# Kernel optimization log

Measured on AMD Instinct MI355X. Metric: run time of the kernel, lower is better.

Reference implementation:

```python
import jax, jax.numpy as jnp
import numpy as np

N, M, D = 65536, 1024, 2

def setup_inputs() -> dict:
    key = jax.random.key(0)
    k1, k2, k3, k4 = jax.random.split(key, 4)
    sample = jax.random.normal(k1, (N, D), dtype=jnp.float32)
    mu = jax.random.uniform(k2, (M, D), dtype=jnp.float32)
    A = jax.random.normal(k3, (M, D, D), dtype=jnp.float32)
    w = jax.random.normal(k4, (M, 1), dtype=jnp.float32)
    return {"sample": sample, "mu": mu, "A": A, "w": w}


def reference(sample, mu, A, w):
    # Covariance-like precision matrices: gamma_j = A_j A_j^T / 2, shape [M, D, D]
    gamma = jnp.matmul(A, jnp.swapaxes(A, 1, 2)) / 2.0
    # Hand-rolled 2x2 determinants (matches covariances_determinants)
    dets = gamma[:, 0, 0] * gamma[:, 1, 1] - gamma[:, 0, 1] * gamma[:, 1, 0]  # [M]
    # log of the scalar factor in front of each Gaussian (weights_log)
    log_w = jax.nn.log_softmax(w, axis=0)[:, 0] + 0.5 * jnp.log(dets)  # [M]
    # Pairwise Mahalanobis quadratic form q_ij = (x_i - mu_j)^T gamma_j (x_i - mu_j)
    diff = sample[:, None, :] - mu[None, :, :]  # [N, M, D]
    q = jnp.einsum('nmd,mde,nme->nm', diff, gamma, diff)  # [N, M]
    # 'lse' mode of kernel_product: log sum_j exp(log_w_j - q_ij)
    ll = jax.scipy.special.logsumexp(log_w[None, :] - q, axis=1)  # [N]
    return ll[:, None]
```

## Files before the change

### kernel.cpp

```cpp
#include <hip/hip_runtime.h>
#include <hip/hip_bf16.h>
#include <math.h>

#define LOG2E 1.4426950408889634f
#define LN2   0.6931471805599453f

typedef float v2f __attribute__((ext_vector_type(2)));

__device__ __forceinline__ float fast_exp2(float x) {
#if __has_builtin(__builtin_amdgcn_exp2f)
    return __builtin_amdgcn_exp2f(x);
#else
    return exp2f(x);
#endif
}

__global__ __launch_bounds__(256) void gm_fused(
        const float* __restrict__ sample,
        const float* __restrict__ mu,
        const float* __restrict__ A,
        const float* __restrict__ w,
        float* __restrict__ out) {
    __shared__ float4 COEF4[1536];
    __shared__ float RED4[4];
    __shared__ float SRED[256];

    const int tid  = threadIdx.x;
    const int lane = tid & 63;
    const int wid  = tid >> 6;

    const int i = blockIdx.x * 64 + lane;
    const float2 xy = ((const float2*)sample)[i];
    const float x = xy.x, y = xy.y;
    const v2f Xv = {x, x}, Yv = {y, y};
    const v2f X2 = {x*x, x*x}, XY = {x*y, x*y}, Y2 = {y*y, y*y};

    const float4 wv = ((const float4*)w)[tid];
    const float wj[4] = {wv.x, wv.y, wv.z, wv.w};

    float v = fmaxf(fmaxf(wv.x, wv.y), fmaxf(wv.z, wv.w));
    #pragma unroll
    for (int o = 32; o; o >>= 1) v = fmaxf(v, __shfl_xor(v, o));
    if (lane == 0) RED4[wid] = v;
    __syncthreads();
    const float wmax = fmaxf(fmaxf(RED4[0], RED4[1]), fmaxf(RED4[2], RED4[3]));
    __syncthreads();

    v = expf(wv.x - wmax) + expf(wv.y - wmax) + expf(wv.z - wmax) + expf(wv.w - wmax);
    #pragma unroll
    for (int o = 32; o; o >>= 1) v += __shfl_xor(v, o);
    if (lane == 0) RED4[wid] = v;
    __syncthreads();
    const float lse = wmax + logf(RED4[0] + RED4[1] + RED4[2] + RED4[3]);
    __syncthreads();

    float lw2[4], G00[4], G2[4], G11[4], MX[4], MY[4];
    #pragma unroll
    for (int k = 0; k < 4; k++) {
        const int j = 4 * tid + k;
        const float4 a = ((const float4*)A)[j];
        const float g00 = 0.5f * (a.x*a.x + a.y*a.y);
        const float g01 = 0.5f * (a.x*a.z + a.y*a.w);
        const float g11 = 0.5f * (a.z*a.z + a.w*a.w);
        const float det = g00*g11 - g01*g01;
        lw2[k] = ((wj[k] - lse) + 0.5f * logf(det)) * LOG2E;
        G00[k] = g00 * LOG2E;
        G2[k]  = 2.f * g01 * LOG2E;
        G11[k] = g11 * LOG2E;
        const float2 m = ((const float2*)mu)[j];
        MX[k] = m.x; MY[k] = m.y;
    }

    v = fmaxf(fmaxf(lw2[0], lw2[1]), fmaxf(lw2[2], lw2[3]));
    #pragma unroll
    for (int o = 32; o; o >>= 1) v = fmaxf(v, __shfl_xor(v, o));
    if (lane == 0) RED4[wid] = v;
    __syncthreads();
    const float Lmax = fmaxf(fmaxf(RED4[0], RED4[1]), fmaxf(RED4[2], RED4[3]));

    #pragma unroll
    for (int kk = 0; kk < 2; kk++) {
        const int k0 = 2*kk, k1 = 2*kk + 1;
        float c0[2], c1[2], c2[2];
        #pragma unroll
        for (int h = 0; h < 2; h++) {
            const int k = k0 + h;
            c1[h] = 2.f*G00[k]*MX[k] + G2[k]*MY[k];
            c2[h] = G2[k]*MX[k] + 2.f*G11[k]*MY[k];
            c0[h] = lw2[k] - (G00[k]*MX[k]*MX[k] + G2[k]*MX[k]*MY[k]
                              + G11[k]*MY[k]*MY[k]) - Lmax;
        }
        const int p = 2 * tid + kk;
        COEF4[3*p + 0] = make_float4(c0[0], c0[1], c1[0], c1[1]);
        COEF4[3*p + 1] = make_float4(c2[0], c2[1], -G00[k0], -G00[k1]);
        COEF4[3*p + 2] = make_float4(-G2[k0], -G2[k1], -G11[k0], -G11[k1]);
    }
    __syncthreads();

    const int part = __builtin_amdgcn_readfirstlane(wid);
    const float4* cp = COEF4 + part * 384;

    float s0 = 0.f, s1 = 0.f, s2 = 0.f, s3 = 0.f;

    for (int p = 0; p < 128; p += 2) {
        const float4 f0 = cp[0], f1 = cp[1], f2 = cp[2];
        const float4 f3 = cp[3], f4 = cp[4], f5 = cp[5];
        cp += 6;

        v2f tA = __builtin_elementwise_fma((v2f){f0.z, f0.w}, Xv, (v2f){f0.x, f0.y});
        tA = __builtin_elementwise_fma((v2f){f1.x, f1.y}, Yv, tA);
        tA = __builtin_elementwise_fma((v2f){f1.z, f1.w}, X2, tA);
        tA = __builtin_elementwise_fma((v2f){f2.x, f2.y}, XY, tA);
        tA = __builtin_elementwise_fma((v2f){f2.z, f2.w}, Y2, tA);

        v2f tB = __builtin_elementwise_fma((v2f){f3.z, f3.w}, Xv, (v2f){f3.x, f3.y});
        tB = __builtin_elementwise_fma((v2f){f4.x, f4.y}, Yv, tB);
        tB = __builtin_elementwise_fma((v2f){f4.z, f4.w}, X2, tB);
        tB = __builtin_elementwise_fma((v2f){f5.x, f5.y}, XY, tB);
        tB = __builtin_elementwise_fma((v2f){f5.z, f5.w}, Y2, tB);

        s0 += fast_exp2(tA.x); s1 += fast_exp2(tA.y);
        s2 += fast_exp2(tB.x); s3 += fast_exp2(tB.y);
    }

    SRED[tid] = (s0 + s1) + (s2 + s3);
    __syncthreads();

    if (tid < 64) {
        float st = SRED[tid] + SRED[tid+64] + SRED[tid+128] + SRED[tid+192];
        float ll;
        if (st >= 1e-30f) {
            ll = LN2 * (Lmax + log2f(st));
        } else {
            float m = -3e38f;
            for (int p = 0; p < 512; p++) {
                const float4 f0 = COEF4[3*p], f1 = COEF4[3*p+1], f2 = COEF4[3*p+2];
                v2f t = __builtin_elementwise_fma((v2f){f0.z, f0.w}, Xv, (v2f){f0.x, f0.y});
                t = __builtin_elementwise_fma((v2f){f1.x, f1.y}, Yv, t);
                t = __builtin_elementwise_fma((v2f){f1.z, f1.w}, X2, t);
                t = __builtin_elementwise_fma((v2f){f2.x, f2.y}, XY, t);
                t = __builtin_elementwise_fma((v2f){f2.z, f2.w}, Y2, t);
                m = fmaxf(m, fmaxf(t.x, t.y));
            }
            float ss = 0.f;
            for (int p = 0; p < 512; p++) {
                const float4 f0 = COEF4[3*p], f1 = COEF4[3*p+1], f2 = COEF4[3*p+2];
                v2f t = __builtin_elementwise_fma((v2f){f0.z, f0.w}, Xv, (v2f){f0.x, f0.y});
                t = __builtin_elementwise_fma((v2f){f1.x, f1.y}, Yv, t);
                t = __builtin_elementwise_fma((v2f){f1.z, f1.w}, X2, t);
                t = __builtin_elementwise_fma((v2f){f2.x, f2.y}, XY, t);
                t = __builtin_elementwise_fma((v2f){f2.z, f2.w}, Y2, t);
                ss += fast_exp2(t.x - m) + fast_exp2(t.y - m);
            }
            ll = LN2 * (Lmax + m + log2f(ss));
        }
        out[i] = ll;
    }
}

extern "C" void kernel_launch(void* const* d_in, const int* in_sizes, int n_in,
                              void* d_out, int out_size, void* d_ws, size_t ws_size,
                              hipStream_t stream) {
    const float* sample = (const float*)d_in[0];
    const float* mu     = (const float*)d_in[1];
    const float* A      = (const float*)d_in[2];
    const float* w      = (const float*)d_in[3];
    float* out = (float*)d_out;

    const int N = in_sizes[0] / 2;

    gm_fused<<<N / 64, 256, 0, stream>>>(sample, mu, A, w, out);
}
```

Measured before the change: 21.64 us.

## Keep mixture coefficients in registers and loop samples with wave reductions

Each lane now loads 16 mixture components' coefficients from shared memory into registers once. Each wave then iterates over 16 samples, fetching each sample with a uniform load and summing across lanes with xor-shuffle reductions. This removes the per-iteration LDS coefficient reads and the final cross-wave shared-memory reduction. The quadratic form is rewritten in a nested Horner-style form. The trade-off is a six-step shuffle reduction per sample, higher register pressure from 96 coefficient values, and sequential sample processing within each wave.

```diff
diff --git a/kernel.cpp b/kernel.cpp
--- a/kernel.cpp
+++ b/kernel.cpp
@@ -21,22 +21,14 @@
         const float* __restrict__ A,
         const float* __restrict__ w,
         float* __restrict__ out) {
-    __shared__ float4 COEF4[1536];
+    __shared__ float COEF[1024 * 6];
     __shared__ float RED4[4];
-    __shared__ float SRED[256];
 
     const int tid  = threadIdx.x;
     const int lane = tid & 63;
     const int wid  = tid >> 6;
 
-    const int i = blockIdx.x * 64 + lane;
-    const float2 xy = ((const float2*)sample)[i];
-    const float x = xy.x, y = xy.y;
-    const v2f Xv = {x, x}, Yv = {y, y};
-    const v2f X2 = {x*x, x*x}, XY = {x*y, x*y}, Y2 = {y*y, y*y};
-
     const float4 wv = ((const float4*)w)[tid];
-    const float wj[4] = {wv.x, wv.y, wv.z, wv.w};
 
     float v = fmaxf(fmaxf(wv.x, wv.y), fmaxf(wv.z, wv.w));
     #pragma unroll
@@ -54,7 +46,8 @@
     const float lse = wmax + logf(RED4[0] + RED4[1] + RED4[2] + RED4[3]);
     __syncthreads();
 
-    float lw2[4], G00[4], G2[4], G11[4], MX[4], MY[4];
+    const float wj[4] = {wv.x, wv.y, wv.z, wv.w};
+    float lw2[4], G00[4], G2[4], G11[4], MXa[4], MYa[4];
     #pragma unroll
     for (int k = 0; k < 4; k++) {
         const int j = 4 * tid + k;
@@ -68,7 +61,7 @@
         G2[k]  = 2.f * g01 * LOG2E;
         G11[k] = g11 * LOG2E;
         const float2 m = ((const float2*)mu)[j];
-        MX[k] = m.x; MY[k] = m.y;
+        MXa[k] = m.x; MYa[k] = m.y;
     }
 
     v = fmaxf(fmaxf(lw2[0], lw2[1]), fmaxf(lw2[2], lw2[3]));
@@ -79,83 +72,88 @@
     const float Lmax = fmaxf(fmaxf(RED4[0], RED4[1]), fmaxf(RED4[2], RED4[3]));
 
     #pragma unroll
-    for (int kk = 0; kk < 2; kk++) {
-        const int k0 = 2*kk, k1 = 2*kk + 1;
-        float c0[2], c1[2], c2[2];
-        #pragma unroll
-        for (int h = 0; h < 2; h++) {
-            const int k = k0 + h;
-            c1[h] = 2.f*G00[k]*MX[k] + G2[k]*MY[k];
-            c2[h] = G2[k]*MX[k] + 2.f*G11[k]*MY[k];
-            c0[h] = lw2[k] - (G00[k]*MX[k]*MX[k] + G2[k]*MX[k]*MY[k]
-                              + G11[k]*MY[k]*MY[k]) - Lmax;
-        }
-        const int p = 2 * tid + kk;
-        COEF4[3*p + 0] = make_float4(c0[0], c0[1], c1[0], c1[1]);
-        COEF4[3*p + 1] = make_float4(c2[0], c2[1], -G00[k0], -G00[k1]);
-        COEF4[3*p + 2] = make_float4(-G2[k0], -G2[k1], -G11[k0], -G11[k1]);
+    for (int k = 0; k < 4; k++) {
+        const int j = 4 * tid + k;
+        const float mx = MXa[k], my = MYa[k];
+        const float c1 = 2.f*G00[k]*mx + G2[k]*my;
+        const float c2 = G2[k]*mx + 2.f*G11[k]*my;
+        const float c0 = lw2[k] - (G00[k]*mx*mx + G2[k]*mx*my + G11[k]*my*my) - Lmax;
+        float* p = &COEF[j * 6];
+        p[0] = c0;      p[1] = c1;     p[2] = c2;
+        p[3] = -G00[k]; p[4] = -G2[k]; p[5] = -G11[k];
     }
     __syncthreads();
 
-    const int part = __builtin_amdgcn_readfirstlane(wid);
-    const float4* cp = COEF4 + part * 384;
-
-    float s0 = 0.f, s1 = 0.f, s2 = 0.f, s3 = 0.f;
-
-    for (int p = 0; p < 128; p += 2) {
-        const float4 f0 = cp[0], f1 = cp[1], f2 = cp[2];
-        const float4 f3 = cp[3], f4 = cp[4], f5 = cp[5];
-        cp += 6;
-
-        v2f tA = __builtin_elementwise_fma((v2f){f0.z, f0.w}, Xv, (v2f){f0.x, f0.y});
-        tA = __builtin_elementwise_fma((v2f){f1.x, f1.y}, Yv, tA);
-        tA = __builtin_elementwise_fma((v2f){f1.z, f1.w}, X2, tA);
-        tA = __builtin_elementwise_fma((v2f){f2.x, f2.y}, XY, tA);
-        tA = __builtin_elementwise_fma((v2f){f2.z, f2.w}, Y2, tA);
-
-        v2f tB = __builtin_elementwise_fma((v2f){f3.z, f3.w}, Xv, (v2f){f3.x, f3.y});
-        tB = __builtin_elementwise_fma((v2f){f4.x, f4.y}, Yv, tB);
-        tB = __builtin_elementwise_fma((v2f){f4.z, f4.w}, X2, tB);
-        tB = __builtin_elementwise_fma((v2f){f5.x, f5.y}, XY, tB);
-        tB = __builtin_elementwise_fma((v2f){f5.z, f5.w}, Y2, tB);
-
-        s0 += fast_exp2(tA.x); s1 += fast_exp2(tA.y);
-        s2 += fast_exp2(tB.x); s3 += fast_exp2(tB.y);
+    v2f C0[8], C1[8], C2[8], D0[8], D1[8], D2[8];
+    #pragma unroll
+    for (int k = 0; k < 8; k++) {
+        const float* pa = &COEF[(lane + 128*k) * 6];
+        const float* pb = &COEF[(lane + 128*k + 64) * 6];
+        C0[k] = (v2f){pa[0], pb[0]};
+        C1[k] = (v2f){pa[1], pb[1]};
+        C2[k] = (v2f){pa[2], pb[2]};
+        D0[k] = (v2f){pa[3], pb[3]};
+        D1[k] = (v2f){pa[4], pb[4]};
+        D2[k] = (v2f){pa[5], pb[5]};
     }
 
-    SRED[tid] = (s0 + s1) + (s2 + s3);
-    __syncthreads();
+    const int sbase = blockIdx.x * 64 + wid * 16;
+    const int ubase = __builtin_amdgcn_readfirstlane(sbase);
+    float myout = 0.f;
 
-    if (tid < 64) {
-        float st = SRED[tid] + SRED[tid+64] + SRED[tid+128] + SRED[tid+192];
+    for (int s = 0; s < 16; ++s) {
+        const float2 xy = ((const float2*)sample)[ubase + s];
+        const float x = xy.x, y = xy.y;
+        const v2f Xv = {x, x}, Yv = {y, y};
+
+        v2f sv = {0.f, 0.f};
+        #pragma unroll
+        for (int k = 0; k < 8; k++) {
+            v2f i1 = __builtin_elementwise_fma(D0[k], Xv, C1[k]);
+            i1     = __builtin_elementwise_fma(D1[k], Yv, i1);
+            v2f i2 = __builtin_elementwise_fma(D2[k], Yv, C2[k]);
+            v2f t  = __builtin_elementwise_fma(i1, Xv, C0[k]);
+            t      = __builtin_elementwise_fma(i2, Yv, t);
+            sv.x += fast_exp2(t.x);
+            sv.y += fast_exp2(t.y);
+        }
+        float st = sv.x + sv.y;
+        #pragma unroll
+        for (int o = 32; o; o >>= 1) st += __shfl_xor(st, o);
+
         float ll;
         if (st >= 1e-30f) {
             ll = LN2 * (Lmax + log2f(st));
         } else {
             float m = -3e38f;
-            for (int p = 0; p < 512; p++) {
-                const float4 f0 = COEF4[3*p], f1 = COEF4[3*p+1], f2 = COEF4[3*p+2];
-                v2f t = __builtin_elementwise_fma((v2f){f0.z, f0.w}, Xv, (v2f){f0.x, f0.y});
-                t = __builtin_elementwise_fma((v2f){f1.x, f1.y}, Yv, t);
-                t = __builtin_elementwise_fma((v2f){f1.z, f1.w}, X2, t);
-                t = __builtin_elementwise_fma((v2f){f2.x, f2.y}, XY, t);
-                t = __builtin_elementwise_fma((v2f){f2.z, f2.w}, Y2, t);
+            #pragma unroll
+            for (int k = 0; k < 8; k++) {
+                v2f i1 = __builtin_elementwise_fma(D0[k], Xv, C1[k]);
+                i1     = __builtin_elementwise_fma(D1[k], Yv, i1);
+                v2f i2 = __builtin_elementwise_fma(D2[k], Yv, C2[k]);
+                v2f t  = __builtin_elementwise_fma(i1, Xv, C0[k]);
+                t      = __builtin_elementwise_fma(i2, Yv, t);
                 m = fmaxf(m, fmaxf(t.x, t.y));
             }
+            #pragma unroll
+            for (int o = 32; o; o >>= 1) m = fmaxf(m, __shfl_xor(m, o));
             float ss = 0.f;
-            for (int p = 0; p < 512; p++) {
-                const float4 f0 = COEF4[3*p], f1 = COEF4[3*p+1], f2 = COEF4[3*p+2];
-                v2f t = __builtin_elementwise_fma((v2f){f0.z, f0.w}, Xv, (v2f){f0.x, f0.y});
-                t = __builtin_elementwise_fma((v2f){f1.x, f1.y}, Yv, t);
-                t = __builtin_elementwise_fma((v2f){f1.z, f1.w}, X2, t);
-                t = __builtin_elementwise_fma((v2f){f2.x, f2.y}, XY, t);
-                t = __builtin_elementwise_fma((v2f){f2.z, f2.w}, Y2, t);
+            #pragma unroll
+            for (int k = 0; k < 8; k++) {
+                v2f i1 = __builtin_elementwise_fma(D0[k], Xv, C1[k]);
+                i1     = __builtin_elementwise_fma(D1[k], Yv, i1);
+                v2f i2 = __builtin_elementwise_fma(D2[k], Yv, C2[k]);
+                v2f t  = __builtin_elementwise_fma(i1, Xv, C0[k]);
+                t      = __builtin_elementwise_fma(i2, Yv, t);
                 ss += fast_exp2(t.x - m) + fast_exp2(t.y - m);
             }
+            #pragma unroll
+            for (int o = 32; o; o >>= 1) ss += __shfl_xor(ss, o);
             ll = LN2 * (Lmax + m + log2f(ss));
         }
-        out[i] = ll;
+        if (lane == s) myout = ll;
     }
+    if (lane < 16) out[sbase + lane] = myout;
 }
 
 extern "C" void kernel_launch(void* const* d_in, const int* in_sizes, int n_in,
```

After: 28.27 us. 1.31x slower.
